# Kernel tuning notes

Hardware: AMD Instinct MI355X
Metric: run time of the kernel (lower is better)

The kernel has to match this reference:

```python
import jax, jax.numpy as jnp
import numpy as np

NOISE_STD = 0.05
ALPHA = 0.2
B, T, I, H, O = 64, 1000, 16, 512, 8


def setup_inputs() -> dict:
    key = jax.random.key(0)
    ks = jax.random.split(key, 5)
    x = jax.random.normal(ks[0], (B, T, I), dtype=jnp.float32)
    noise = jax.random.normal(ks[1], (B, T, H), dtype=jnp.float32)
    # parameter init mirrors torch: wi ~ N(0,1), wrec ~ N(0, rho/sqrt(H)), wo ~ N(0, 1/H)
    wi = jax.random.normal(ks[2], (I, H), dtype=jnp.float32)
    si = jnp.ones((I,), dtype=jnp.float32)
    wrec = jax.random.normal(ks[3], (H, H), dtype=jnp.float32) * (1.0 / np.sqrt(H))
    wo = jax.random.normal(ks[4], (H, O), dtype=jnp.float32) * (1.0 / H)
    so = jnp.ones((O,), dtype=jnp.float32)
    h0 = jnp.zeros((H,), dtype=jnp.float32)
    return {"x": x, "noise": noise, "wi": wi, "si": si, "wrec": wrec,
            "wo": wo, "so": so, "h0": h0}


def reference(x, noise, wi, si, wrec, wo, so, h0):
    # proxy params: wi_full = (wi.T * si).T ; wo_full = wo * so
    wi_full = si[:, None] * wi            # (I, H)
    wo_full = wo * so                      # (H, O)
    # input projection is time-parallel; hoist out of the scan
    x_proj = jnp.einsum('bti,ih->bth', x, wi_full)  # (B, T, H)

    def step(h, inp):
        xp, nz = inp                       # (B, H) each
        r = jnp.tanh(h)
        h_new = h + NOISE_STD * nz + ALPHA * (-h + r @ wrec.T + xp)
        out_t = jnp.tanh(h_new) @ wo_full  # (B, O)
        return h_new, out_t

    h_init = jnp.broadcast_to(h0, (x.shape[0], h0.shape[0]))
    _, out = jax.lax.scan(step, h_init,
                          (jnp.swapaxes(x_proj, 0, 1), jnp.swapaxes(noise, 0, 1)))
    return jnp.swapaxes(out, 0, 1)         # (B, T, O)
```

## Files before the change

### kernel.cpp

```cpp
#include <hip/hip_runtime.h>

#define BB 64
#define TT 1000
#define II 16
#define HH 512
#define OO 8
#define NOISE_STD 0.05f
#define ALPHA 0.2f

#define NGROUPS 32
#define BPG 2
#define NSLABS 8
#define JS 64
#define NTHREADS 512
#define NBLOCKS (NGROUPS * NSLABS)


__global__ void __launch_bounds__(NTHREADS, 1) rnn_kernel(
    const float* __restrict__ x, const float* __restrict__ noise,
    const float* __restrict__ wi, const float* __restrict__ si,
    const float* __restrict__ wrec, const float* __restrict__ wo,
    const float* __restrict__ so, const float* __restrict__ h0,
    float* __restrict__ out, unsigned long long* rtag)
{
    __shared__ __align__(16) float rlds[2][BPG][HH];
    __shared__ __align__(16) float zpart[2][NSLABS][BPG][JS];
    __shared__ __align__(16) float xpbuf[2][BPG][JS];

    const int tid  = threadIdx.x;
    const int lane = tid & 63;
    const int wid  = tid >> 6;

    const int xcd  = blockIdx.x & 7;
    const int bidx = blockIdx.x >> 3;
    const int grp  = xcd * 4 + (bidx >> 3);
    const int slab = bidx & 7;
    const int gb   = grp * BPG;
    const int j0   = slab * JS;

    float w_reg[64];
    {
        const float4* wrow = (const float4*)(wrec + (size_t)(j0 + lane) * HH + wid * 64);
        #pragma unroll
        for (int c = 0; c < 16; ++c) {
            float4 v = wrow[c];
            w_reg[4*c+0] = v.x; w_reg[4*c+1] = v.y;
            w_reg[4*c+2] = v.z; w_reg[4*c+3] = v.w;
        }
    }

    float hreg = 0.f;
    if (wid < BPG) hreg = h0[j0 + lane];

    float wiF_r[16];
    if (wid >= 6) {
        #pragma unroll
        for (int i = 0; i < 16; ++i) wiF_r[i] = si[i] * wi[i * HH + j0 + lane];
    }
    float wo_r[8][8];
    if (wid == 4 || wid == 5) {
        float so_[8];
        #pragma unroll
        for (int o = 0; o < 8; ++o) so_[o] = so[o];
        #pragma unroll
        for (int m = 0; m < 8; ++m) {
            const float4* wrow = (const float4*)(wo + (size_t)(lane + 64 * m) * OO);
            float4 wa = wrow[0], wb2 = wrow[1];
            wo_r[m][0] = wa.x  * so_[0]; wo_r[m][1] = wa.y  * so_[1];
            wo_r[m][2] = wa.z  * so_[2]; wo_r[m][3] = wa.w  * so_[3];
            wo_r[m][4] = wb2.x * so_[4]; wo_r[m][5] = wb2.y * so_[5];
            wo_r[m][6] = wb2.z * so_[6]; wo_r[m][7] = wb2.w * so_[7];
        }
    }

    unsigned int rb0, rb1;
    {
        float rv = tanhf(h0[wid * 64 + lane]);
        rb0 = __float_as_uint(rv);
        rb1 = rb0;
        rlds[0][0][wid * 64 + lane] = rv;
        rlds[0][1][wid * 64 + lane] = rv;
    }
    if (wid >= 6) {
        const int b = wid - 6;
        const float4* xb = (const float4*)(x + ((size_t)(gb + b) * TT + 0) * II);
        float4 x0 = xb[0], x1 = xb[1], x2 = xb[2], x3 = xb[3];
        xpbuf[0][b][lane] =
              x0.x*wiF_r[0]  + x0.y*wiF_r[1]  + x0.z*wiF_r[2]  + x0.w*wiF_r[3]
            + x1.x*wiF_r[4]  + x1.y*wiF_r[5]  + x1.z*wiF_r[6]  + x1.w*wiF_r[7]
            + x2.x*wiF_r[8]  + x2.y*wiF_r[9]  + x2.z*wiF_r[10] + x2.w*wiF_r[11]
            + x3.x*wiF_r[12] + x3.y*wiF_r[13] + x3.z*wiF_r[14] + x3.w*wiF_r[15];
    }
    __syncthreads();

    for (int t = 0; t < TT; ++t) {
        const int par = t & 1;
        const int nxt = (t + 1) & 1;

        float nz = 0.f;
        if (wid < BPG)
            nz = noise[((size_t)(gb + wid) * TT + t) * HH + j0 + lane];

        if (t > 0) {
            const unsigned long long* s0 =
                rtag + (size_t)par * (BB * HH) + (size_t)gb * HH + wid * 64 + lane;
            unsigned long long v0, v1;
            const unsigned int tg = (unsigned int)t;
            do {
                v0 = __hip_atomic_load(s0,      __ATOMIC_RELAXED, __HIP_MEMORY_SCOPE_AGENT);
                v1 = __hip_atomic_load(s0 + HH, __ATOMIC_RELAXED, __HIP_MEMORY_SCOPE_AGENT);
            } while ((unsigned int)(v0 >> 32) != tg || (unsigned int)(v1 >> 32) != tg);
            rb0 = (unsigned int)v0;
            rb1 = (unsigned int)v1;
            rlds[par][0][wid * 64 + lane] = __uint_as_float(rb0);
            rlds[par][1][wid * 64 + lane] = __uint_as_float(rb1);
        }

        float a0 = 0.f, a1 = 0.f;
        #pragma unroll
        for (int c = 0; c < 64; ++c) {
            float r0 = __uint_as_float(__builtin_amdgcn_readlane(rb0, c));
            float r1 = __uint_as_float(__builtin_amdgcn_readlane(rb1, c));
            a0 += w_reg[c] * r0;
            a1 += w_reg[c] * r1;
        }
        zpart[par][wid][0][lane] = a0;
        zpart[par][wid][1][lane] = a1;
        __syncthreads();

        if (wid < BPG) {
            float z = 0.f;
            #pragma unroll
            for (int k8 = 0; k8 < 8; ++k8) z += zpart[par][k8][wid][lane];
            float xp = xpbuf[par][wid][lane];
            float hn = hreg + NOISE_STD * nz + ALPHA * (z + xp - hreg);
            hreg = hn;
            float rnew = tanhf(hn);
            unsigned long long pv =
                ((unsigned long long)(unsigned int)(t + 1) << 32)
              | (unsigned long long)__float_as_uint(rnew);
            __hip_atomic_store(rtag + (size_t)nxt * (BB * HH)
                                    + (size_t)(gb + wid) * HH + j0 + lane,
                               pv, __ATOMIC_RELAXED, __HIP_MEMORY_SCOPE_AGENT);
        } else if (wid == 4 || wid == 5) {
            const int b = wid - 4;
            if (t > 0) {
                float acc0=0.f,acc1=0.f,acc2=0.f,acc3=0.f,
                      acc4=0.f,acc5=0.f,acc6=0.f,acc7=0.f;
                #pragma unroll
                for (int m = 0; m < 8; ++m) {
                    float rv = rlds[par][b][lane + 64 * m];
                    acc0 += rv * wo_r[m][0]; acc1 += rv * wo_r[m][1];
                    acc2 += rv * wo_r[m][2]; acc3 += rv * wo_r[m][3];
                    acc4 += rv * wo_r[m][4]; acc5 += rv * wo_r[m][5];
                    acc6 += rv * wo_r[m][6]; acc7 += rv * wo_r[m][7];
                }
                float res = 0.f;
                #define RED_(A, O) { float v_ = A; \
                    v_ += __shfl_xor(v_, 1);  v_ += __shfl_xor(v_, 2); \
                    v_ += __shfl_xor(v_, 4);  v_ += __shfl_xor(v_, 8); \
                    v_ += __shfl_xor(v_, 16); v_ += __shfl_xor(v_, 32); \
                    if (lane == O) res = v_; }
                RED_(acc0, 0) RED_(acc1, 1) RED_(acc2, 2) RED_(acc3, 3)
                RED_(acc4, 4) RED_(acc5, 5) RED_(acc6, 6) RED_(acc7, 7)
                #undef RED_
                if (lane < 8)
                    out[((size_t)(gb + b) * TT + (t - 1)) * OO + lane] = res;
            }
        } else if (wid >= 6) {
            const int b = wid - 6;
            if (t + 1 < TT) {
                const float4* xb =
                    (const float4*)(x + ((size_t)(gb + b) * TT + (t + 1)) * II);
                float4 x0 = xb[0], x1 = xb[1], x2 = xb[2], x3 = xb[3];
                xpbuf[nxt][b][lane] =
                      x0.x*wiF_r[0]  + x0.y*wiF_r[1]  + x0.z*wiF_r[2]  + x0.w*wiF_r[3]
                    + x1.x*wiF_r[4]  + x1.y*wiF_r[5]  + x1.z*wiF_r[6]  + x1.w*wiF_r[7]
                    + x2.x*wiF_r[8]  + x2.y*wiF_r[9]  + x2.z*wiF_r[10] + x2.w*wiF_r[11]
                    + x3.x*wiF_r[12] + x3.y*wiF_r[13] + x3.z*wiF_r[14] + x3.w*wiF_r[15];
            }
        }
    }

    {
        const unsigned long long* s0 =
            rtag + (size_t)gb * HH + wid * 64 + lane;
        unsigned long long v0, v1;
        const unsigned int tg = (unsigned int)TT;
        do {
            v0 = __hip_atomic_load(s0,      __ATOMIC_RELAXED, __HIP_MEMORY_SCOPE_AGENT);
            v1 = __hip_atomic_load(s0 + HH, __ATOMIC_RELAXED, __HIP_MEMORY_SCOPE_AGENT);
        } while ((unsigned int)(v0 >> 32) != tg || (unsigned int)(v1 >> 32) != tg);
        rlds[0][0][wid * 64 + lane] = __uint_as_float((unsigned int)v0);
        rlds[0][1][wid * 64 + lane] = __uint_as_float((unsigned int)v1);
    }
    __syncthreads();
    if (wid == 4 || wid == 5) {
        const int b = wid - 4;
        float acc0=0.f,acc1=0.f,acc2=0.f,acc3=0.f,acc4=0.f,acc5=0.f,acc6=0.f,acc7=0.f;
        #pragma unroll
        for (int m = 0; m < 8; ++m) {
            float rv = rlds[0][b][lane + 64 * m];
            acc0 += rv * wo_r[m][0]; acc1 += rv * wo_r[m][1];
            acc2 += rv * wo_r[m][2]; acc3 += rv * wo_r[m][3];
            acc4 += rv * wo_r[m][4]; acc5 += rv * wo_r[m][5];
            acc6 += rv * wo_r[m][6]; acc7 += rv * wo_r[m][7];
        }
        float res = 0.f;
        #define RED_(A, O) { float v_ = A; \
            v_ += __shfl_xor(v_, 1);  v_ += __shfl_xor(v_, 2); \
            v_ += __shfl_xor(v_, 4);  v_ += __shfl_xor(v_, 8); \
            v_ += __shfl_xor(v_, 16); v_ += __shfl_xor(v_, 32); \
            if (lane == O) res = v_; }
        RED_(acc0, 0) RED_(acc1, 1) RED_(acc2, 2) RED_(acc3, 3)
        RED_(acc4, 4) RED_(acc5, 5) RED_(acc6, 6) RED_(acc7, 7)
        #undef RED_
        if (lane < 8)
            out[((size_t)(gb + b) * TT + (TT - 1)) * OO + lane] = res;
    }
}

extern "C" void kernel_launch(void* const* d_in, const int* in_sizes, int n_in,
                              void* d_out, int out_size, void* d_ws, size_t ws_size,
                              hipStream_t stream) {
    const float* x     = (const float*)d_in[0];
    const float* noise = (const float*)d_in[1];
    const float* wi    = (const float*)d_in[2];
    const float* si    = (const float*)d_in[3];
    const float* wrec  = (const float*)d_in[4];
    const float* wo    = (const float*)d_in[5];
    const float* so    = (const float*)d_in[6];
    const float* h0    = (const float*)d_in[7];
    float* out = (float*)d_out;
    unsigned long long* rtag = (unsigned long long*)d_ws;

    (void)in_sizes; (void)n_in; (void)out_size; (void)ws_size;

    void* args[] = {(void*)&x, (void*)&noise, (void*)&wi, (void*)&si,
                    (void*)&wrec, (void*)&wo, (void*)&so, (void*)&h0,
                    (void*)&out, (void*)&rtag};
    hipLaunchCooperativeKernel((void*)rnn_kernel, dim3(NBLOCKS), dim3(NTHREADS),
                               args, 0, stream);
}
```

Measured before the change: 1.992 ms.

## Fuse output projection into recurrent readlane loop and spread state update across waves

The output projection is folded into the per-step readlane loop: each wave accumulates partial W_o dot-products alongside the recurrent matvec and reduces them through a small LDS buffer, which removes the rlds staging buffer and the shuffle-based reduction done by dedicated waves. The hidden-state update now runs on 16 lanes in each of the 8 waves instead of 64 lanes in 2 waves, and the input projection is computed inline instead of by separate waves. The next step's tagged values are speculatively preloaded after publishing, and a lighter barrier that waits only on LDS replaces __syncthreads. The cost is extra FMAs and registers per step and a partial-lane update path.

```diff
diff --git a/kernel.cpp b/kernel.cpp
--- a/kernel.cpp
+++ b/kernel.cpp
@@ -16,6 +16,16 @@
 #define NBLOCKS (NGROUPS * NSLABS)
 
 
+#define AGENT_LD(P)   __hip_atomic_load((P), __ATOMIC_RELAXED, __HIP_MEMORY_SCOPE_AGENT)
+#define AGENT_ST(P,V) __hip_atomic_store((P), (V), __ATOMIC_RELAXED, __HIP_MEMORY_SCOPE_AGENT)
+
+#define BAR() do { \
+    asm volatile("s_waitcnt lgkmcnt(0)" ::: "memory"); \
+    __builtin_amdgcn_sched_barrier(0); \
+    __builtin_amdgcn_s_barrier(); \
+    __builtin_amdgcn_sched_barrier(0); \
+} while (0)
+
 __global__ void __launch_bounds__(NTHREADS, 1) rnn_kernel(
     const float* __restrict__ x, const float* __restrict__ noise,
     const float* __restrict__ wi, const float* __restrict__ si,
@@ -23,9 +33,8 @@
     const float* __restrict__ so, const float* __restrict__ h0,
     float* __restrict__ out, unsigned long long* rtag)
 {
-    __shared__ __align__(16) float rlds[2][BPG][HH];
     __shared__ __align__(16) float zpart[2][NSLABS][BPG][JS];
-    __shared__ __align__(16) float xpbuf[2][BPG][JS];
+    __shared__ __align__(16) float zout[2][NSLABS][BPG][OO];
 
     const int tid  = threadIdx.x;
     const int lane = tid & 63;
@@ -48,29 +57,23 @@
             w_reg[4*c+2] = v.z; w_reg[4*c+3] = v.w;
         }
     }
-
+    const int oo = lane & 7;
+    float wo_reg[64];
+    {
+        const float so_o = so[oo];
+        #pragma unroll 8
+        for (int c = 0; c < 64; ++c)
+            wo_reg[c] = wo[(size_t)(wid * 64 + c) * OO + oo] * so_o;
+    }
+    const int pb   = lane >> 3;
+    const int prow = wid * 8 + (lane & 7);
+    const int jrow = j0 + prow;
     float hreg = 0.f;
-    if (wid < BPG) hreg = h0[j0 + lane];
-
     float wiF_r[16];
-    if (wid >= 6) {
-        #pragma unroll
-        for (int i = 0; i < 16; ++i) wiF_r[i] = si[i] * wi[i * HH + j0 + lane];
-    }
-    float wo_r[8][8];
-    if (wid == 4 || wid == 5) {
-        float so_[8];
-        #pragma unroll
-        for (int o = 0; o < 8; ++o) so_[o] = so[o];
-        #pragma unroll
-        for (int m = 0; m < 8; ++m) {
-            const float4* wrow = (const float4*)(wo + (size_t)(lane + 64 * m) * OO);
-            float4 wa = wrow[0], wb2 = wrow[1];
-            wo_r[m][0] = wa.x  * so_[0]; wo_r[m][1] = wa.y  * so_[1];
-            wo_r[m][2] = wa.z  * so_[2]; wo_r[m][3] = wa.w  * so_[3];
-            wo_r[m][4] = wb2.x * so_[4]; wo_r[m][5] = wb2.y * so_[5];
-            wo_r[m][6] = wb2.z * so_[6]; wo_r[m][7] = wb2.w * so_[7];
-        }
+    if (lane < 16) {
+        hreg = h0[jrow];
+        #pragma unroll
+        for (int i = 0; i < II; ++i) wiF_r[i] = si[i] * wi[i * HH + jrow];
     }
 
     unsigned int rb0, rb1;
@@ -78,145 +81,113 @@
         float rv = tanhf(h0[wid * 64 + lane]);
         rb0 = __float_as_uint(rv);
         rb1 = rb0;
-        rlds[0][0][wid * 64 + lane] = rv;
-        rlds[0][1][wid * 64 + lane] = rv;
-    }
-    if (wid >= 6) {
-        const int b = wid - 6;
-        const float4* xb = (const float4*)(x + ((size_t)(gb + b) * TT + 0) * II);
-        float4 x0 = xb[0], x1 = xb[1], x2 = xb[2], x3 = xb[3];
-        xpbuf[0][b][lane] =
-              x0.x*wiF_r[0]  + x0.y*wiF_r[1]  + x0.z*wiF_r[2]  + x0.w*wiF_r[3]
-            + x1.x*wiF_r[4]  + x1.y*wiF_r[5]  + x1.z*wiF_r[6]  + x1.w*wiF_r[7]
-            + x2.x*wiF_r[8]  + x2.y*wiF_r[9]  + x2.z*wiF_r[10] + x2.w*wiF_r[11]
-            + x3.x*wiF_r[12] + x3.y*wiF_r[13] + x3.z*wiF_r[14] + x3.w*wiF_r[15];
-    }
+    }
+    unsigned long long sp0 = 0, sp1 = 0;
     __syncthreads();
 
     for (int t = 0; t < TT; ++t) {
         const int par = t & 1;
-        const int nxt = (t + 1) & 1;
+        const int nxt = par ^ 1;
 
         float nz = 0.f;
-        if (wid < BPG)
-            nz = noise[((size_t)(gb + wid) * TT + t) * HH + j0 + lane];
+        float4 xv0, xv1, xv2, xv3;
+        if (lane < 16) {
+            nz = noise[((size_t)(gb + pb) * TT + t) * HH + jrow];
+            const float4* xp4 = (const float4*)(x + ((size_t)(gb + pb) * TT + t) * II);
+            xv0 = xp4[0]; xv1 = xp4[1]; xv2 = xp4[2]; xv3 = xp4[3];
+        }
 
         if (t > 0) {
             const unsigned long long* s0 =
                 rtag + (size_t)par * (BB * HH) + (size_t)gb * HH + wid * 64 + lane;
-            unsigned long long v0, v1;
+            const unsigned long long* s1 = s0 + HH;
             const unsigned int tg = (unsigned int)t;
-            do {
-                v0 = __hip_atomic_load(s0,      __ATOMIC_RELAXED, __HIP_MEMORY_SCOPE_AGENT);
-                v1 = __hip_atomic_load(s0 + HH, __ATOMIC_RELAXED, __HIP_MEMORY_SCOPE_AGENT);
-            } while ((unsigned int)(v0 >> 32) != tg || (unsigned int)(v1 >> 32) != tg);
+            unsigned long long v0 = sp0, v1 = sp1;
+            while ((unsigned int)(v0 >> 32) != tg || (unsigned int)(v1 >> 32) != tg) {
+                v0 = AGENT_LD(s0);
+                v1 = AGENT_LD(s1);
+            }
             rb0 = (unsigned int)v0;
             rb1 = (unsigned int)v1;
-            rlds[par][0][wid * 64 + lane] = __uint_as_float(rb0);
-            rlds[par][1][wid * 64 + lane] = __uint_as_float(rb1);
-        }
-
-        float a0 = 0.f, a1 = 0.f;
+        }
+
+        float a0 = 0.f, a1 = 0.f, po0 = 0.f, po1 = 0.f;
         #pragma unroll
         for (int c = 0; c < 64; ++c) {
             float r0 = __uint_as_float(__builtin_amdgcn_readlane(rb0, c));
             float r1 = __uint_as_float(__builtin_amdgcn_readlane(rb1, c));
-            a0 += w_reg[c] * r0;
-            a1 += w_reg[c] * r1;
+            a0  += w_reg[c]  * r0;
+            a1  += w_reg[c]  * r1;
+            po0 += wo_reg[c] * r0;
+            po1 += wo_reg[c] * r1;
         }
         zpart[par][wid][0][lane] = a0;
         zpart[par][wid][1][lane] = a1;
-        __syncthreads();
-
-        if (wid < BPG) {
+        if (lane < 16)
+            zout[par][wid][pb][oo] = pb ? po1 : po0;
+        BAR();
+
+        if (lane < 16) {
             float z = 0.f;
             #pragma unroll
-            for (int k8 = 0; k8 < 8; ++k8) z += zpart[par][k8][wid][lane];
-            float xp = xpbuf[par][wid][lane];
+            for (int w8 = 0; w8 < NSLABS; ++w8) z += zpart[par][w8][pb][prow];
+            float xp = xv0.x*wiF_r[0]  + xv0.y*wiF_r[1]  + xv0.z*wiF_r[2]  + xv0.w*wiF_r[3]
+                     + xv1.x*wiF_r[4]  + xv1.y*wiF_r[5]  + xv1.z*wiF_r[6]  + xv1.w*wiF_r[7]
+                     + xv2.x*wiF_r[8]  + xv2.y*wiF_r[9]  + xv2.z*wiF_r[10] + xv2.w*wiF_r[11]
+                     + xv3.x*wiF_r[12] + xv3.y*wiF_r[13] + xv3.z*wiF_r[14] + xv3.w*wiF_r[15];
             float hn = hreg + NOISE_STD * nz + ALPHA * (z + xp - hreg);
             hreg = hn;
             float rnew = tanhf(hn);
-            unsigned long long pv =
-                ((unsigned long long)(unsigned int)(t + 1) << 32)
-              | (unsigned long long)__float_as_uint(rnew);
-            __hip_atomic_store(rtag + (size_t)nxt * (BB * HH)
-                                    + (size_t)(gb + wid) * HH + j0 + lane,
-                               pv, __ATOMIC_RELAXED, __HIP_MEMORY_SCOPE_AGENT);
-        } else if (wid == 4 || wid == 5) {
-            const int b = wid - 4;
-            if (t > 0) {
-                float acc0=0.f,acc1=0.f,acc2=0.f,acc3=0.f,
-                      acc4=0.f,acc5=0.f,acc6=0.f,acc7=0.f;
-                #pragma unroll
-                for (int m = 0; m < 8; ++m) {
-                    float rv = rlds[par][b][lane + 64 * m];
-                    acc0 += rv * wo_r[m][0]; acc1 += rv * wo_r[m][1];
-                    acc2 += rv * wo_r[m][2]; acc3 += rv * wo_r[m][3];
-                    acc4 += rv * wo_r[m][4]; acc5 += rv * wo_r[m][5];
-                    acc6 += rv * wo_r[m][6]; acc7 += rv * wo_r[m][7];
-                }
-                float res = 0.f;
-                #define RED_(A, O) { float v_ = A; \
-                    v_ += __shfl_xor(v_, 1);  v_ += __shfl_xor(v_, 2); \
-                    v_ += __shfl_xor(v_, 4);  v_ += __shfl_xor(v_, 8); \
-                    v_ += __shfl_xor(v_, 16); v_ += __shfl_xor(v_, 32); \
-                    if (lane == O) res = v_; }
-                RED_(acc0, 0) RED_(acc1, 1) RED_(acc2, 2) RED_(acc3, 3)
-                RED_(acc4, 4) RED_(acc5, 5) RED_(acc6, 6) RED_(acc7, 7)
-                #undef RED_
-                if (lane < 8)
-                    out[((size_t)(gb + b) * TT + (t - 1)) * OO + lane] = res;
-            }
-        } else if (wid >= 6) {
-            const int b = wid - 6;
-            if (t + 1 < TT) {
-                const float4* xb =
-                    (const float4*)(x + ((size_t)(gb + b) * TT + (t + 1)) * II);
-                float4 x0 = xb[0], x1 = xb[1], x2 = xb[2], x3 = xb[3];
-                xpbuf[nxt][b][lane] =
-                      x0.x*wiF_r[0]  + x0.y*wiF_r[1]  + x0.z*wiF_r[2]  + x0.w*wiF_r[3]
-                    + x1.x*wiF_r[4]  + x1.y*wiF_r[5]  + x1.z*wiF_r[6]  + x1.w*wiF_r[7]
-                    + x2.x*wiF_r[8]  + x2.y*wiF_r[9]  + x2.z*wiF_r[10] + x2.w*wiF_r[11]
-                    + x3.x*wiF_r[12] + x3.y*wiF_r[13] + x3.z*wiF_r[14] + x3.w*wiF_r[15];
-            }
-        }
-    }
-
-    {
+            AGENT_ST(rtag + (size_t)nxt * (BB * HH) + (size_t)(gb + pb) * HH + jrow,
+                     ((unsigned long long)(unsigned int)(t + 1) << 32)
+                   | (unsigned long long)__float_as_uint(rnew));
+        }
+
+        {
+            const unsigned long long* sn =
+                rtag + (size_t)nxt * (BB * HH) + (size_t)gb * HH + wid * 64 + lane;
+            sp0 = AGENT_LD(sn);
+            sp1 = AGENT_LD(sn + HH);
+        }
+
+        if (t > 0 && wid == (t & 7) && lane < 16) {
+            float s = 0.f;
+            #pragma unroll
+            for (int w8 = 0; w8 < NSLABS; ++w8) s += zout[par][w8][pb][oo];
+            out[((size_t)(gb + pb) * TT + (t - 1)) * OO + oo] = s;
+        }
+    }
+
+    {
+        const int par = TT & 1;
         const unsigned long long* s0 =
-            rtag + (size_t)gb * HH + wid * 64 + lane;
-        unsigned long long v0, v1;
+            rtag + (size_t)par * (BB * HH) + (size_t)gb * HH + wid * 64 + lane;
+        const unsigned long long* s1 = s0 + HH;
         const unsigned int tg = (unsigned int)TT;
-        do {
-            v0 = __hip_atomic_load(s0,      __ATOMIC_RELAXED, __HIP_MEMORY_SCOPE_AGENT);
-            v1 = __hip_atomic_load(s0 + HH, __ATOMIC_RELAXED, __HIP_MEMORY_SCOPE_AGENT);
-        } while ((unsigned int)(v0 >> 32) != tg || (unsigned int)(v1 >> 32) != tg);
-        rlds[0][0][wid * 64 + lane] = __uint_as_float((unsigned int)v0);
-        rlds[0][1][wid * 64 + lane] = __uint_as_float((unsigned int)v1);
-    }
-    __syncthreads();
-    if (wid == 4 || wid == 5) {
-        const int b = wid - 4;
-        float acc0=0.f,acc1=0.f,acc2=0.f,acc3=0.f,acc4=0.f,acc5=0.f,acc6=0.f,acc7=0.f;
-        #pragma unroll
-        for (int m = 0; m < 8; ++m) {
-            float rv = rlds[0][b][lane + 64 * m];
-            acc0 += rv * wo_r[m][0]; acc1 += rv * wo_r[m][1];
-            acc2 += rv * wo_r[m][2]; acc3 += rv * wo_r[m][3];
-            acc4 += rv * wo_r[m][4]; acc5 += rv * wo_r[m][5];
-            acc6 += rv * wo_r[m][6]; acc7 += rv * wo_r[m][7];
-        }
-        float res = 0.f;
-        #define RED_(A, O) { float v_ = A; \
-            v_ += __shfl_xor(v_, 1);  v_ += __shfl_xor(v_, 2); \
-            v_ += __shfl_xor(v_, 4);  v_ += __shfl_xor(v_, 8); \
-            v_ += __shfl_xor(v_, 16); v_ += __shfl_xor(v_, 32); \
-            if (lane == O) res = v_; }
-        RED_(acc0, 0) RED_(acc1, 1) RED_(acc2, 2) RED_(acc3, 3)
-        RED_(acc4, 4) RED_(acc5, 5) RED_(acc6, 6) RED_(acc7, 7)
-        #undef RED_
-        if (lane < 8)
-            out[((size_t)(gb + b) * TT + (TT - 1)) * OO + lane] = res;
+        unsigned long long v0 = sp0, v1 = sp1;
+        while ((unsigned int)(v0 >> 32) != tg || (unsigned int)(v1 >> 32) != tg) {
+            v0 = AGENT_LD(s0);
+            v1 = AGENT_LD(s1);
+        }
+        rb0 = (unsigned int)v0;
+        rb1 = (unsigned int)v1;
+        float po0 = 0.f, po1 = 0.f;
+        #pragma unroll
+        for (int c = 0; c < 64; ++c) {
+            float r0 = __uint_as_float(__builtin_amdgcn_readlane(rb0, c));
+            float r1 = __uint_as_float(__builtin_amdgcn_readlane(rb1, c));
+            po0 += wo_reg[c] * r0;
+            po1 += wo_reg[c] * r1;
+        }
+        if (lane < 16)
+            zout[par][wid][pb][oo] = pb ? po1 : po0;
+        BAR();
+        if (wid == (TT & 7) && lane < 16) {
+            float s = 0.f;
+            #pragma unroll
+            for (int w8 = 0; w8 < NSLABS; ++w8) s += zout[par][w8][pb][oo];
+            out[((size_t)(gb + pb) * TT + (TT - 1)) * OO + oo] = s;
+        }
     }
 }
 
```

Result: slower. 4.853 ms (+143.6%).
